# Kernel tuning notes

Hardware: AMD Instinct MI355X
Metric: run time of the kernel (lower is better)

The kernel has to match this reference:

```python
import jax, jax.numpy as jnp
import numpy as np
from jax import lax

B, N, K = 8, 4096, 64
RATIO1, R1 = 0.5, 0.2
RATIO2, R2 = 0.25, 0.4
SA1_DIMS = [3, 32, 32, 64]
SA2_DIMS = [64 + 3, 64, 64, 128]
SA3_DIMS = [128 + 3, 128, 256, 512]


def _mlp_params(key, dims, prefix):
    params = {}
    for i, (din, dout) in enumerate(zip(dims[:-1], dims[1:])):
        key, k1 = jax.random.split(key)
        s = 1.0 / np.sqrt(din)
        params[f"{prefix}_w{i}"] = jax.random.uniform(k1, (din, dout), jnp.float32, -s, s)
        params[f"{prefix}_b{i}"] = jnp.zeros((dout,), jnp.float32)
    return params, key


def setup_inputs() -> dict:
    key = jax.random.key(0)
    key, kp = jax.random.split(key)
    inp = {"pos": jax.random.uniform(kp, (B, N, 3), jnp.float32)}  # unit-cube point clouds
    p1, key = _mlp_params(key, SA1_DIMS, "sa1"); inp.update(p1)
    p2, key = _mlp_params(key, SA2_DIMS, "sa2"); inp.update(p2)
    p3, key = _mlp_params(key, SA3_DIMS, "sa3"); inp.update(p3)
    key, k1, k2 = jax.random.split(key, 3)
    s = 1.0 / np.sqrt(512)
    inp["w_mu"] = jax.random.uniform(k1, (512, 32), jnp.float32, -s, s)
    inp["b_mu"] = jnp.zeros((32,), jnp.float32)
    inp["w_lv"] = jax.random.uniform(k2, (512, 32), jnp.float32, -s, s)
    inp["b_lv"] = jnp.zeros((32,), jnp.float32)
    return inp


def _mlp(x, params):
    # PyG MLP semantics (plain_last=True): ReLU on all but the final layer.
    for i, (w, b) in enumerate(params):
        x = x @ w + b
        if i < len(params) - 1:
            x = jax.nn.relu(x)
    return x


def _fps(pos, M):
    # Farthest point sampling, deterministic start at index 0. pos: [N,3] -> [M]
    n = pos.shape[0]
    def step(carry, _):
        dist, far = carry
        d = jnp.sum((pos - pos[far]) ** 2, axis=-1)
        dist = jnp.minimum(dist, d)
        return (dist, jnp.argmax(dist).astype(jnp.int32)), far
    _, idx = lax.scan(step, (jnp.full(n, jnp.inf, pos.dtype), jnp.int32(0)), None, length=M)
    return idx


def _sa(x, pos, ratio, r, params):
    # SAModule: FPS -> radius query (K nearest within r) -> gather -> MLP -> masked max
    Nn = pos.shape[1]
    M = int(round(ratio * Nn))
    idx = jax.vmap(lambda p: _fps(p, M))(pos)                 # [B,M]
    centers = jax.vmap(lambda p, i: p[i])(pos, idx)           # [B,M,3]
    d2 = jnp.sum((centers[:, :, None, :] - pos[:, None, :, :]) ** 2, axis=-1)  # [B,M,N]
    neg = jnp.where(d2 <= r * r, -d2, -jnp.inf)
    vals, nbr = lax.top_k(neg, K)                             # [B,M,K]
    mask = vals > -jnp.inf                                    # valid neighbors (self always valid)
    pos_j = jax.vmap(lambda p, i: p[i])(pos, nbr)             # [B,M,K,3]
    rel = pos_j - centers[:, :, None, :]
    if x is None:
        feat = rel
    else:
        x_j = jax.vmap(lambda f, i: f[i])(x, nbr)             # [B,M,K,C]
        feat = jnp.concatenate([x_j, rel], axis=-1)
    h = _mlp(feat, params)                                    # [B,M,K,C']
    h = jnp.where(mask[..., None], h, -jnp.inf)
    out = jnp.max(h, axis=2)                                  # scatter-max aggregation
    out = jnp.where(jnp.isfinite(out), out, 0.0)
    return out, centers


def reference(pos, sa1_w0, sa1_b0, sa1_w1, sa1_b1, sa1_w2, sa1_b2,
              sa2_w0, sa2_b0, sa2_w1, sa2_b1, sa2_w2, sa2_b2,
              sa3_w0, sa3_b0, sa3_w1, sa3_b1, sa3_w2, sa3_b2,
              w_mu, b_mu, w_lv, b_lv):
    p1 = [(sa1_w0, sa1_b0), (sa1_w1, sa1_b1), (sa1_w2, sa1_b2)]
    p2 = [(sa2_w0, sa2_b0), (sa2_w1, sa2_b1), (sa2_w2, sa2_b2)]
    p3 = [(sa3_w0, sa3_b0), (sa3_w1, sa3_b1), (sa3_w2, sa3_b2)]
    x1, pos1 = _sa(None, pos, RATIO1, R1, p1)                 # [B,2048,64]
    x2, pos2 = _sa(x1, pos1, RATIO2, R2, p2)                  # [B,512,128]
    g = _mlp(jnp.concatenate([x2, pos2], axis=-1), p3)        # [B,512,512]
    feat = jnp.max(g, axis=1)                                 # global max pool [B,512]
    mu = feat @ w_mu + b_mu
    log_var = feat @ w_lv + b_lv
    eps = jax.random.normal(jax.random.key(42), mu.shape, mu.dtype)
    z = mu + eps * jnp.exp(0.5 * log_var)
    return (z, mu, log_var)
```

## Files before the change

kernel.cpp:

```cpp
#include <hip/hip_runtime.h>
#include <cstdint>
#include <cstddef>


constexpr int BATCH = 8;
constexpr int NPT0  = 4096;
constexpr int M1    = 2048;
constexpr int M2    = 512;
constexpr int KNB   = 64;
constexpr int CAP   = 1024;
constexpr int NCONS = 248;

constexpr size_t O_WT1S1 = 0;
constexpr size_t O_WT2S1 = 96;
constexpr size_t O_WT3S1 = 1120;
constexpr size_t O_WT1S2 = 3168;
constexpr size_t O_WT2S2 = 7456;
constexpr size_t O_WT3S2 = 11552;
constexpr size_t O_WT1S3 = 19744;
constexpr size_t O_WT2S3 = 36512;
constexpr size_t O_POS1  = 69280;
constexpr size_t O_X1    = 118432;
constexpr size_t O_POS2  = 1167008;
constexpr size_t O_X2    = 1179296;
constexpr size_t O_H2G   = O_X1;
constexpr size_t O_FP    = O_X2;
constexpr size_t O_PROG  = 1703584;

template <int C>
__device__ __forceinline__ int dppmov(int x) {
  return __builtin_amdgcn_update_dpp(x, x, C, 0xF, 0xF, false);
}

__device__ __forceinline__ float wave_fmax_scal(float x) {
  x = fmaxf(x, __int_as_float(dppmov<0x111>(__float_as_int(x))));
  x = fmaxf(x, __int_as_float(dppmov<0x112>(__float_as_int(x))));
  x = fmaxf(x, __int_as_float(dppmov<0x114>(__float_as_int(x))));
  x = fmaxf(x, __int_as_float(dppmov<0x118>(__float_as_int(x))));
  x = fmaxf(x, __int_as_float(dppmov<0x142>(__float_as_int(x))));
  x = fmaxf(x, __int_as_float(dppmov<0x143>(__float_as_int(x))));
  return __int_as_float(__builtin_amdgcn_readlane(__float_as_int(x), 63));
}

template <int C>
__device__ __forceinline__ void dpp_key_max(uint32_t& lo, uint32_t& hi) {
  uint32_t olo = (uint32_t)dppmov<C>((int)lo);
  uint32_t ohi = (uint32_t)dppmov<C>((int)hi);
  bool bet = (ohi > hi) || (ohi == hi && olo > lo);
  lo = bet ? olo : lo;
  hi = bet ? ohi : hi;
}
__device__ __forceinline__ void wave_key_max_scal(uint32_t& lo, uint32_t& hi) {
  dpp_key_max<0x111>(lo, hi);
  dpp_key_max<0x112>(lo, hi);
  dpp_key_max<0x114>(lo, hi);
  dpp_key_max<0x118>(lo, hi);
  dpp_key_max<0x142>(lo, hi);
  dpp_key_max<0x143>(lo, hi);
  lo = (uint32_t)__builtin_amdgcn_readlane((int)lo, 63);
  hi = (uint32_t)__builtin_amdgcn_readlane((int)hi, 63);
}
template <int C>
__device__ __forceinline__ void dpp_key_min(uint32_t& lo, uint32_t& hi) {
  uint32_t olo = (uint32_t)dppmov<C>((int)lo);
  uint32_t ohi = (uint32_t)dppmov<C>((int)hi);
  bool bet = (ohi < hi) || (ohi == hi && olo < lo);
  lo = bet ? olo : lo;
  hi = bet ? ohi : hi;
}
__device__ __forceinline__ void wave_key_min_scal(uint32_t& lo, uint32_t& hi) {
  dpp_key_min<0x111>(lo, hi);
  dpp_key_min<0x112>(lo, hi);
  dpp_key_min<0x114>(lo, hi);
  dpp_key_min<0x118>(lo, hi);
  dpp_key_min<0x142>(lo, hi);
  dpp_key_min<0x143>(lo, hi);
  lo = (uint32_t)__builtin_amdgcn_readlane((int)lo, 63);
  hi = (uint32_t)__builtin_amdgcn_readlane((int)hi, 63);
}

__device__ __forceinline__ void wave_lds_fence() {
  asm volatile("s_waitcnt lgkmcnt(0)" ::: "memory");
}

__device__ __forceinline__ uint32_t rotl32(uint32_t x, int d) {
  return (x << d) | (x >> (32 - d));
}

__device__ __forceinline__ void threefry_0_42(uint32_t c0, uint32_t c1,
                                              uint32_t& o0, uint32_t& o1) {
  const uint32_t k0 = 0u, k1 = 42u;
  const uint32_t ks[3] = {k0, k1, k0 ^ k1 ^ 0x1BD11BDAu};
  uint32_t x0 = c0 + ks[0];
  uint32_t x1 = c1 + ks[1];
  const int R0[4] = {13, 15, 26, 6};
  const int R1[4] = {17, 29, 16, 24};
  #pragma unroll
  for (int g = 0; g < 5; ++g) {
    const int* R = (g & 1) ? R1 : R0;
    #pragma unroll
    for (int r = 0; r < 4; ++r) {
      x0 += x1;
      x1 = rotl32(x1, R[r]);
      x1 ^= x0;
    }
    x0 += ks[(g + 1) % 3];
    x1 += ks[(g + 2) % 3] + (uint32_t)(g + 1);
  }
  o0 = x0; o1 = x1;
}

__device__ __forceinline__ float erfinv_xla(float x) {
  float w = -log1pf(-x * x);
  float p;
  if (w < 5.0f) {
    w = w - 2.5f;
    p = 2.81022636e-08f;
    p = fmaf(p, w, 3.43273939e-07f);
    p = fmaf(p, w, -3.5233877e-06f);
    p = fmaf(p, w, -4.39150654e-06f);
    p = fmaf(p, w, 0.00021858087f);
    p = fmaf(p, w, -0.00125372503f);
    p = fmaf(p, w, -0.00417768164f);
    p = fmaf(p, w, 0.246640727f);
    p = fmaf(p, w, 1.50140941f);
  } else {
    w = sqrtf(w) - 3.0f;
    p = -0.000200214257f;
    p = fmaf(p, w, 0.000100950558f);
    p = fmaf(p, w, 0.00134934322f);
    p = fmaf(p, w, -0.00367342844f);
    p = fmaf(p, w, 0.00573950773f);
    p = fmaf(p, w, -0.0076224613f);
    p = fmaf(p, w, 0.00943887047f);
    p = fmaf(p, w, 1.00167406f);
    p = fmaf(p, w, 2.83297682f);
  }
  return p * x;
}

__global__ __launch_bounds__(256) void prep_transpose(
    const float* __restrict__ a0, const float* __restrict__ a1,
    const float* __restrict__ a2, const float* __restrict__ a3,
    const float* __restrict__ a4, const float* __restrict__ a5,
    const float* __restrict__ a6, const float* __restrict__ a7,
    float* __restrict__ ws) {
  int u0 = blockIdx.x * 256 + threadIdx.x;
  if (u0 < 16) ((int*)(ws + O_PROG))[u0] = 0;
  int u = u0;
  if (u < 96)    { ws[O_WT1S1 + u] = a0[(u % 3)   * 32  + u / 3];   return; } u -= 96;
  if (u < 1024)  { ws[O_WT2S1 + u] = a1[(u % 32)  * 32  + u / 32];  return; } u -= 1024;
  if (u < 2048)  { ws[O_WT3S1 + u] = a2[(u % 32)  * 64  + u / 32];  return; } u -= 2048;
  if (u < 4288)  { ws[O_WT1S2 + u] = a3[(u % 67)  * 64  + u / 67];  return; } u -= 4288;
  if (u < 4096)  { ws[O_WT2S2 + u] = a4[(u % 64)  * 64  + u / 64];  return; } u -= 4096;
  if (u < 8192)  { ws[O_WT3S2 + u] = a5[(u % 64)  * 128 + u / 64];  return; } u -= 8192;
  if (u < 16768) { ws[O_WT1S3 + u] = a6[(u % 131) * 128 + u / 131]; return; } u -= 16768;
  if (u < 32768) { ws[O_WT2S3 + u] = a7[(u % 128) * 256 + u / 128]; return; }
}

template <int N, int M, int T>
__device__ __forceinline__ void fps_body(const float* __restrict__ pos,
                                         float* __restrict__ centers,
                                         int* __restrict__ prog,
                                         char* smem, int b) {
  constexpr int PPT = N / T;
  constexpr int NW  = T / 64;
  float* px = (float*)smem;
  float* py = px + N;
  float* pz = py + N;
  int*    tags  = (int*)(pz + N);
  float4* slotA = (float4*)(tags + 16);
  float*  slotZ = (float*)(slotA + 2 * NW);
  const int tid  = threadIdx.x;
  const int lane = tid & 63;
  const int wid  = tid >> 6;
  const float* pb = pos + (size_t)b * N * 3;

  if (tid < 16) tags[tid] = -1;

  float mx[PPT], my[PPT], mz[PPT], md[PPT];
  #pragma unroll
  for (int s = 0; s < PPT; ++s) {
    int i = s * T + tid;
    float x = pb[i * 3 + 0], y = pb[i * 3 + 1], z = pb[i * 3 + 2];
    px[i] = x; py[i] = y; pz[i] = z;
    mx[s] = x; my[s] = y; mz[s] = z;
    md[s] = __builtin_inff();
  }
  __syncthreads();

  float cx = px[0], cy = py[0], cz = pz[0];
  float* cb = centers + (size_t)b * M * 3;

  for (int m = 0; m < M; ++m) {
    if (tid == 0) {
      cb[m * 3 + 0] = cx; cb[m * 3 + 1] = cy; cb[m * 3 + 2] = cz;
      if ((m & 63) == 63)
        __hip_atomic_store(prog + b, m + 1, __ATOMIC_RELEASE,
                           __HIP_MEMORY_SCOPE_AGENT);
    }
    float bv = -1.0f;
    int   bi = 0x7FFFFFFF;
    {
      #pragma clang fp contract(off)
      #pragma unroll
      for (int s = 0; s < PPT; ++s) {
        float dx = mx[s] - cx, dy = my[s] - cy, dz = mz[s] - cz;
        float d = (dx * dx + dy * dy) + dz * dz;
        float nd = fminf(md[s], d);
        md[s] = nd;
        if (nd > bv) { bv = nd; bi = s * T + tid; }
      }
    }
    uint32_t klo = ~(uint32_t)bi;
    uint32_t khi = __float_as_uint(bv);
    wave_key_max_scal(klo, khi);
    int p = (int)~klo;

    float wx = px[p], wy = py[p], wz = pz[p];
    const int par = (m & 1) * NW;
    if (lane == 0) {
      slotA[par + wid] =
          make_float4(__uint_as_float(khi), __uint_as_float(klo), wx, wy);
      slotZ[par + wid] = wz;
    }
    __builtin_amdgcn_fence(__ATOMIC_RELEASE, "workgroup");
    if (lane == 0)
      __hip_atomic_store(&tags[wid], m, __ATOMIC_RELAXED,
                         __HIP_MEMORY_SCOPE_WORKGROUP);
    for (;;) {
      int tmin = __hip_atomic_load(&tags[0], __ATOMIC_RELAXED,
                                   __HIP_MEMORY_SCOPE_WORKGROUP);
      #pragma unroll
      for (int w = 1; w < NW; ++w) {
        int tw = __hip_atomic_load(&tags[w], __ATOMIC_RELAXED,
                                   __HIP_MEMORY_SCOPE_WORKGROUP);
        tmin = min(tmin, tw);
      }
      if (tmin >= m) break;
    }
    __builtin_amdgcn_fence(__ATOMIC_ACQUIRE, "workgroup");

    float4 aw0 = slotA[par + 0];
    uint32_t Khi = __float_as_uint(aw0.x), Klo = __float_as_uint(aw0.y);
    float sx = aw0.z, sy = aw0.w, sz = slotZ[par + 0];
    #pragma unroll
    for (int w = 1; w < NW; ++w) {
      float4 aw = slotA[par + w];
      float zz = slotZ[par + w];
      uint32_t ohi = __float_as_uint(aw.x), olo = __float_as_uint(aw.y);
      bool bet = (ohi > Khi) || (ohi == Khi && olo > Klo);
      Khi = bet ? ohi : Khi;
      Klo = bet ? olo : Klo;
      sx  = bet ? aw.z : sx;
      sy  = bet ? aw.w : sy;
      sz  = bet ? zz   : sz;
    }
    cx = sx; cy = sy; cz = sz;
  }
}

template <int NPTS, int DF, int D1, int D2, int DOUT, int MM>
__device__ __forceinline__ void sa_body(
    const float* __restrict__ pts, const float* __restrict__ feats,
    const float* __restrict__ centers, float* __restrict__ outf,
    const float* __restrict__ wt1, const float* __restrict__ bz1,
    const float* __restrict__ wt2, const float* __restrict__ bz2,
    const float* __restrict__ wt3, const float* __restrict__ bz3,
    float r2max, int* __restrict__ prog, char* smem) {
  constexpr int DIN = DF + 3;
  const int lane = threadIdx.x & 63;
  const int wid  = threadIdx.x >> 6;
  const int g0 = ((int)blockIdx.x - 8) * 8 + wid;
  const int b = g0 & 7;
  const int mbase = g0 >> 3;
  float* sd = (float*)(smem + wid * 8192);
  int*   si = (int*)(smem + wid * 8192 + 4096);
  const float* pb = pts + (size_t)b * NPTS * 3;

  for (int m = mbase; m < MM; m += NCONS) {
    for (;;) {
      int r = 0;
      if (lane == 0)
        r = __hip_atomic_load(prog + b, __ATOMIC_ACQUIRE,
                              __HIP_MEMORY_SCOPE_AGENT);
      r = __builtin_amdgcn_readfirstlane(r);
      if (r > m) break;
      if (m - r > 128) __builtin_amdgcn_s_sleep(64);
      else             __builtin_amdgcn_s_sleep(4);
    }
    __builtin_amdgcn_fence(__ATOMIC_ACQUIRE, "agent");

    const float* cc = centers + ((size_t)b * MM + m) * 3;
    const float cx = cc[0], cy = cc[1], cz = cc[2];

    int cnt = 0;
    const unsigned long long ltmask = (1ull << lane) - 1ull;
    for (int base = 0; base < NPTS; base += 64) {
      int i = base + lane;
      float x3 = pb[i * 3 + 0], y3 = pb[i * 3 + 1], z3 = pb[i * 3 + 2];
      float d2;
      {
        #pragma clang fp contract(off)
        float dx = cx - x3, dy = cy - y3, dz = cz - z3;
        d2 = (dx * dx + dy * dy) + dz * dz;
      }
      bool inr = (d2 <= r2max);
      unsigned long long mk = __ballot(inr);
      int p = cnt + (int)__popcll(mk & ltmask);
      if (inr && p < CAP) { sd[p] = d2; si[p] = i; }
      cnt += (int)__popcll(mk);
    }
    if (cnt > CAP) cnt = CAP;
    wave_lds_fence();

    int my_nbr = -1;
    if (cnt <= KNB) {
      my_nbr = (lane < cnt) ? si[lane] : -1;
    } else {
      constexpr int SMAX = CAP / 64;
      float rd[SMAX];
      #pragma unroll
      for (int s = 0; s < SMAX; ++s) {
        rd[s] = __builtin_inff();
        if (s * 64 < cnt) {
          int q = s * 64 + lane;
          if (q < cnt) rd[s] = sd[q];
        }
      }
      for (int k = 0; k < KNB; ++k) {
        float bv = rd[0];
        int   bp = lane;
        #pragma unroll
        for (int s = 1; s < SMAX; ++s) {
          if (s * 64 < cnt) {
            if (rd[s] < bv) { bv = rd[s]; bp = s * 64 + lane; }
          }
        }
        uint32_t klo = (uint32_t)bp;
        uint32_t khi = __float_as_uint(bv);
        wave_key_min_scal(klo, khi);
        int bpw = (int)klo;
        if (lane == k) my_nbr = si[bpw];
        int wl = bpw & 63, wsl = bpw >> 6;
        #pragma unroll
        for (int s = 0; s < SMAX; ++s) {
          if (s * 64 < cnt) {
            rd[s] = (lane == wl && s == wsl) ? __builtin_inff() : rd[s];
          }
        }
      }
    }
    const bool valid = (my_nbr >= 0);
    const int safeN = valid ? my_nbr : 0;

    float rel[3];
    {
      const float* pr = pb + (size_t)safeN * 3;
      rel[0] = pr[0] - cx; rel[1] = pr[1] - cy; rel[2] = pr[2] - cz;
    }
    float xin[DF > 0 ? DF : 1];
    if constexpr (DF > 0) {
      const float* xr = feats + ((size_t)b * NPTS + safeN) * DF;
      #pragma unroll
      for (int i = 0; i < DF; i += 4) {
        float4 v = *reinterpret_cast<const float4*>(xr + i);
        xin[i] = v.x; xin[i + 1] = v.y; xin[i + 2] = v.z; xin[i + 3] = v.w;
      }
    }

    float h1[D1];
    for (int c = 0; c < D1; c += 4) {
      const float* w0 = wt1 + (c + 0) * DIN;
      const float* w1 = wt1 + (c + 1) * DIN;
      const float* w2 = wt1 + (c + 2) * DIN;
      const float* w3 = wt1 + (c + 3) * DIN;
      float a0 = bz1[c + 0], a1 = bz1[c + 1], a2 = bz1[c + 2], a3 = bz1[c + 3];
      if constexpr (DF > 0) {
        #pragma unroll
        for (int i = 0; i < DF; ++i) {
          a0 = fmaf(xin[i], w0[i], a0);
          a1 = fmaf(xin[i], w1[i], a1);
          a2 = fmaf(xin[i], w2[i], a2);
          a3 = fmaf(xin[i], w3[i], a3);
        }
      }
      #pragma unroll
      for (int r = 0; r < 3; ++r) {
        a0 = fmaf(rel[r], w0[DF + r], a0);
        a1 = fmaf(rel[r], w1[DF + r], a1);
        a2 = fmaf(rel[r], w2[DF + r], a2);
        a3 = fmaf(rel[r], w3[DF + r], a3);
      }
      h1[c + 0] = fmaxf(a0, 0.0f);
      h1[c + 1] = fmaxf(a1, 0.0f);
      h1[c + 2] = fmaxf(a2, 0.0f);
      h1[c + 3] = fmaxf(a3, 0.0f);
    }

    float h2[D2];
    for (int c = 0; c < D2; c += 4) {
      const float* w0 = wt2 + (c + 0) * D1;
      const float* w1 = wt2 + (c + 1) * D1;
      const float* w2 = wt2 + (c + 2) * D1;
      const float* w3 = wt2 + (c + 3) * D1;
      float a0 = bz2[c + 0], a1 = bz2[c + 1], a2 = bz2[c + 2], a3 = bz2[c + 3];
      #pragma unroll
      for (int i = 0; i < D1; ++i) {
        a0 = fmaf(h1[i], w0[i], a0);
        a1 = fmaf(h1[i], w1[i], a1);
        a2 = fmaf(h1[i], w2[i], a2);
        a3 = fmaf(h1[i], w3[i], a3);
      }
      h2[c + 0] = fmaxf(a0, 0.0f);
      h2[c + 1] = fmaxf(a1, 0.0f);
      h2[c + 2] = fmaxf(a2, 0.0f);
      h2[c + 3] = fmaxf(a3, 0.0f);
    }

    float* orow = outf + ((size_t)b * MM + m) * DOUT;
    #pragma unroll
    for (int u = 0; u < DOUT / 64; ++u) {
      float outv = 0.0f;
      for (int ccb = 0; ccb < 64; ccb += 4) {
        const int c = u * 64 + ccb;
        const float* w0 = wt3 + (c + 0) * D2;
        const float* w1 = wt3 + (c + 1) * D2;
        const float* w2 = wt3 + (c + 2) * D2;
        const float* w3 = wt3 + (c + 3) * D2;
        float a0 = bz3[c + 0], a1 = bz3[c + 1], a2 = bz3[c + 2], a3 = bz3[c + 3];
        #pragma unroll
        for (int i = 0; i < D2; ++i) {
          a0 = fmaf(h2[i], w0[i], a0);
          a1 = fmaf(h2[i], w1[i], a1);
          a2 = fmaf(h2[i], w2[i], a2);
          a3 = fmaf(h2[i], w3[i], a3);
        }
        const float NI = -__builtin_inff();
        float s0 = wave_fmax_scal(valid ? a0 : NI);
        float s1 = wave_fmax_scal(valid ? a1 : NI);
        float s2 = wave_fmax_scal(valid ? a2 : NI);
        float s3 = wave_fmax_scal(valid ? a3 : NI);
        if (lane == ccb + 0) outv = s0;
        if (lane == ccb + 1) outv = s1;
        if (lane == ccb + 2) outv = s2;
        if (lane == ccb + 3) outv = s3;
      }
      orow[u * 64 + lane] = outv;
    }
  }
}

__global__ __launch_bounds__(512, 2) void stageA_kernel(
    const float* __restrict__ pos, float* __restrict__ ws,
    const float* __restrict__ bz1, const float* __restrict__ bz2,
    const float* __restrict__ bz3) {
  extern __shared__ char smem[];
  int* prog = (int*)(ws + O_PROG);
  if (blockIdx.x < 8) {
    asm volatile("s_setprio 3");
    fps_body<NPT0, M1, 512>(pos, ws + O_POS1, prog, smem, blockIdx.x);
  } else {
    sa_body<NPT0, 0, 32, 32, 64, M1>(
        pos, nullptr, ws + O_POS1, ws + O_X1,
        ws + O_WT1S1, bz1, ws + O_WT2S1, bz2, ws + O_WT3S1, bz3,
        0.04f, prog, smem);
  }
}

__global__ __launch_bounds__(512, 2) void stageB_kernel(
    float* __restrict__ ws,
    const float* __restrict__ bz1, const float* __restrict__ bz2,
    const float* __restrict__ bz3) {
  extern __shared__ char smem[];
  int* prog = (int*)(ws + O_PROG) + 8;
  if (blockIdx.x < 8) {
    asm volatile("s_setprio 3");
    fps_body<M1, M2, 512>(ws + O_POS1, ws + O_POS2, prog, smem, blockIdx.x);
  } else {
    sa_body<M1, 64, 64, 64, 128, M2>(
        ws + O_POS1, ws + O_X1, ws + O_POS2, ws + O_X2,
        ws + O_WT1S2, bz1, ws + O_WT2S2, bz2, ws + O_WT3S2, bz3,
        0.16f, prog, smem);
  }
}

__global__ __launch_bounds__(256) void sa3_l12_kernel(
    const float* __restrict__ x2, const float* __restrict__ pos2,
    const float* __restrict__ wt1, const float* __restrict__ bz1,
    const float* __restrict__ wt2, const float* __restrict__ bz2,
    float* __restrict__ h2g) {
  __shared__ float H[64 * 132];
  const int tid = threadIdx.x;
  const int lane = tid & 63, w = tid >> 6;
  const int b = blockIdx.x >> 3, tile = blockIdx.x & 7;
  const int pt = tile * 64 + lane;
  const float* xrow = x2 + ((size_t)b * 512 + pt) * 128;
  float* hrow = H + lane * 132;
  const int c0 = w * 32;

  float f[64];
  #pragma unroll
  for (int i = 0; i < 64; i += 4) {
    float4 v = *reinterpret_cast<const float4*>(xrow + i);
    f[i] = v.x; f[i + 1] = v.y; f[i + 2] = v.z; f[i + 3] = v.w;
  }
  for (int c = c0; c < c0 + 32; ++c) {
    const float* wv = wt1 + c * 131;
    float acc = bz1[c];
    #pragma unroll
    for (int i = 0; i < 64; ++i) acc = fmaf(f[i], wv[i], acc);
    hrow[c] = acc;
  }
  #pragma unroll
  for (int i = 0; i < 64; i += 4) {
    float4 v = *reinterpret_cast<const float4*>(xrow + 64 + i);
    f[i] = v.x; f[i + 1] = v.y; f[i + 2] = v.z; f[i + 3] = v.w;
  }
  float q0, q1, q2;
  {
    const float* pr = pos2 + ((size_t)b * 512 + pt) * 3;
    q0 = pr[0]; q1 = pr[1]; q2 = pr[2];
  }
  for (int c = c0; c < c0 + 32; ++c) {
    const float* wv = wt1 + c * 131 + 64;
    float acc = hrow[c];
    #pragma unroll
    for (int i = 0; i < 64; ++i) acc = fmaf(f[i], wv[i], acc);
    acc = fmaf(q0, wv[64], acc);
    acc = fmaf(q1, wv[65], acc);
    acc = fmaf(q2, wv[66], acc);
    hrow[c] = fmaxf(acc, 0.0f);
  }
  __syncthreads();

  float h[128];
  #pragma unroll
  for (int i = 0; i < 128; i += 4) {
    float4 v = *reinterpret_cast<const float4*>(hrow + i);
    h[i] = v.x; h[i + 1] = v.y; h[i + 2] = v.z; h[i + 3] = v.w;
  }
  float* grow = h2g + ((size_t)b * 512 + pt) * 256;
  const int c1 = w * 64;
  for (int c = c1; c < c1 + 64; ++c) {
    const float* wv = wt2 + c * 128;
    float acc = bz2[c];
    #pragma unroll
    for (int i = 0; i < 128; ++i) acc = fmaf(h[i], wv[i], acc);
    grow[c] = fmaxf(acc, 0.0f);
  }
}

__global__ __launch_bounds__(256) void sa3_l3_kernel(
    const float* __restrict__ h2g, const float* __restrict__ w3,
    const float* __restrict__ bz3, float* __restrict__ fpart) {
  const int tid = threadIdx.x;
  const int blk = blockIdx.x;
  const int b   = blk >> 6;
  const int t16 = (blk >> 1) & 31;
  const int cb  = blk & 1;
  const int c = cb * 256 + tid;
  const float* hbase = h2g + ((size_t)b * 512 + t16 * 16) * 256;

  float acc[16];
  #pragma unroll
  for (int j = 0; j < 16; ++j) acc[j] = 0.0f;

  for (int i0 = 0; i0 < 256; i0 += 8) {
    float wv[8];
    #pragma unroll
    for (int u = 0; u < 8; ++u) wv[u] = w3[(size_t)(i0 + u) * 512 + c];
    #pragma unroll
    for (int j = 0; j < 16; ++j) {
      const float* hr = hbase + (size_t)j * 256 + i0;
      #pragma unroll
      for (int u = 0; u < 8; ++u) acc[j] = fmaf(hr[u], wv[u], acc[j]);
    }
  }
  float mv = acc[0];
  #pragma unroll
  for (int j = 1; j < 16; ++j) mv = fmaxf(mv, acc[j]);
  fpart[((size_t)b * 32 + t16) * 512 + c] = mv + bz3[c];
}

__global__ __launch_bounds__(64) void final_kernel(
    const float* __restrict__ fpart,
    const float* __restrict__ wmu, const float* __restrict__ bmu,
    const float* __restrict__ wlv, const float* __restrict__ blv,
    float* __restrict__ outp) {
  __shared__ float feat[512];
  const int tid = threadIdx.x;
  const int b = blockIdx.x;
  for (int cidx = tid; cidx < 512; cidx += 64) {
    float mv = fpart[(size_t)b * 32 * 512 + cidx];
    #pragma unroll
    for (int t = 1; t < 32; ++t)
      mv = fmaxf(mv, fpart[((size_t)b * 32 + t) * 512 + cidx]);
    feat[cidx] = mv;
  }
  __syncthreads();
  if (tid < 32) {
    const int c = tid;
    double amu = 0.0, alv = 0.0;
    for (int i = 0; i < 512; ++i) {
      double fv = (double)feat[i];
      amu += fv * (double)wmu[i * 32 + c];
      alv += fv * (double)wlv[i * 32 + c];
    }
    float mu = (float)amu + bmu[c];
    float lv = (float)alv + blv[c];

    uint32_t n = (uint32_t)(b * 32 + c);
    uint32_t o0, o1;
    threefry_0_42(0u, n, o0, o1);
    uint32_t bits = o0 ^ o1;
    float fl = __uint_as_float((bits >> 9) | 0x3f800000u) - 1.0f;
    const float LO = -0.99999994039535522461f;
    float u = fl * 2.0f + LO;
    u = fmaxf(LO, u);
    float eps = 1.4142135623730951f * erfinv_xla(u);
    float z = mu + eps * expf(0.5f * lv);

    outp[b * 32 + c] = z;
    outp[256 + b * 32 + c] = mu;
    outp[512 + b * 32 + c] = lv;
  }
}

extern "C" void kernel_launch(void* const* d_in, const int* in_sizes, int n_in,
                              void* d_out, int out_size, void* d_ws, size_t ws_size,
                              hipStream_t stream) {
  (void)in_sizes; (void)n_in; (void)out_size; (void)ws_size;
  const float* pos  = (const float*)d_in[0];
  const float* s1w0 = (const float*)d_in[1];  const float* s1b0 = (const float*)d_in[2];
  const float* s1w1 = (const float*)d_in[3];  const float* s1b1 = (const float*)d_in[4];
  const float* s1w2 = (const float*)d_in[5];  const float* s1b2 = (const float*)d_in[6];
  const float* s2w0 = (const float*)d_in[7];  const float* s2b0 = (const float*)d_in[8];
  const float* s2w1 = (const float*)d_in[9];  const float* s2b1 = (const float*)d_in[10];
  const float* s2w2 = (const float*)d_in[11]; const float* s2b2 = (const float*)d_in[12];
  const float* s3w0 = (const float*)d_in[13]; const float* s3b0 = (const float*)d_in[14];
  const float* s3w1 = (const float*)d_in[15]; const float* s3b1 = (const float*)d_in[16];
  const float* s3w2 = (const float*)d_in[17]; const float* s3b2 = (const float*)d_in[18];
  const float* wmu  = (const float*)d_in[19]; const float* bmu  = (const float*)d_in[20];
  const float* wlv  = (const float*)d_in[21]; const float* blv  = (const float*)d_in[22];
  float* ws = (float*)d_ws;
  float* out = (float*)d_out;

  prep_transpose<<<271, 256, 0, stream>>>(s1w0, s1w1, s1w2, s2w0, s2w1, s2w2,
                                          s3w0, s3w1, ws);

  stageA_kernel<<<8 + NCONS, 512, 65536, stream>>>(pos, ws, s1b0, s1b1, s1b2);

  stageB_kernel<<<8 + NCONS, 512, 65536, stream>>>(ws, s2b0, s2b1, s2b2);

  sa3_l12_kernel<<<BATCH * 8, 256, 0, stream>>>(
      ws + O_X2, ws + O_POS2, ws + O_WT1S3, s3b0, ws + O_WT2S3, s3b1,
      ws + O_H2G);

  sa3_l3_kernel<<<BATCH * 64, 256, 0, stream>>>(ws + O_H2G, s3w2, s3b2,
                                                ws + O_FP);

  final_kernel<<<BATCH, 64, 0, stream>>>(ws + O_FP, wmu, bmu, wlv, blv, out);
}
```

Measured before the change: 3.781 ms.

## Shrink FPS to 4 waves and batch consumer work into contiguous center chunks

The FPS producer now runs its serial loop with 256 threads (4 waves) instead of 512. All 512 threads still cooperatively stage the point cloud into LDS, then the upper half exit. This aims to cut the per-iteration cross-wave reduction and barrier cost on the serial critical path, at the price of more points per thread. Consumer waves now take contiguous chunks of centers (8 in stage A, 2 in stage B), poll the progress counter once per chunk with a relaxed load followed by an acquire fence, and process the chunk's centers back to back. This reduces polling overhead but delays the start of each chunk until its last center has been produced.

```diff
diff --git a/kernel.cpp b/kernel.cpp
--- a/kernel.cpp
+++ b/kernel.cpp
@@ -158,13 +158,14 @@
   if (u < 32768) { ws[O_WT2S3 + u] = a7[(u % 128) * 256 + u / 128]; return; }
 }
 
-template <int N, int M, int T>
+template <int N, int M>
 __device__ __forceinline__ void fps_body(const float* __restrict__ pos,
                                          float* __restrict__ centers,
                                          int* __restrict__ prog,
                                          char* smem, int b) {
-  constexpr int PPT = N / T;
-  constexpr int NW  = T / 64;
+  constexpr int TP  = 256;
+  constexpr int PPT = N / TP;
+  constexpr int NW  = 4;
   float* px = (float*)smem;
   float* py = px + N;
   float* pz = py + N;
@@ -177,17 +178,21 @@
   const float* pb = pos + (size_t)b * N * 3;
 
   if (tid < 16) tags[tid] = -1;
+  for (int i = tid; i < N; i += 512) {
+    px[i] = pb[i * 3 + 0];
+    py[i] = pb[i * 3 + 1];
+    pz[i] = pb[i * 3 + 2];
+  }
+  __syncthreads();
+  if (tid >= TP) return;
 
   float mx[PPT], my[PPT], mz[PPT], md[PPT];
   #pragma unroll
   for (int s = 0; s < PPT; ++s) {
-    int i = s * T + tid;
-    float x = pb[i * 3 + 0], y = pb[i * 3 + 1], z = pb[i * 3 + 2];
-    px[i] = x; py[i] = y; pz[i] = z;
-    mx[s] = x; my[s] = y; mz[s] = z;
+    int i = s * TP + tid;
+    mx[s] = px[i]; my[s] = py[i]; mz[s] = pz[i];
     md[s] = __builtin_inff();
   }
-  __syncthreads();
 
   float cx = px[0], cy = py[0], cz = pz[0];
   float* cb = centers + (size_t)b * M * 3;
@@ -209,7 +214,7 @@
         float d = (dx * dx + dy * dy) + dz * dz;
         float nd = fminf(md[s], d);
         md[s] = nd;
-        if (nd > bv) { bv = nd; bi = s * T + tid; }
+        if (nd > bv) { bv = nd; bi = s * TP + tid; }
       }
     }
     uint32_t klo = ~(uint32_t)bi;
@@ -260,7 +265,7 @@
   }
 }
 
-template <int NPTS, int DF, int D1, int D2, int DOUT, int MM>
+template <int NPTS, int DF, int D1, int D2, int DOUT, int MM, int CH>
 __device__ __forceinline__ void sa_body(
     const float* __restrict__ pts, const float* __restrict__ feats,
     const float* __restrict__ centers, float* __restrict__ outf,
@@ -269,184 +274,189 @@
     const float* __restrict__ wt3, const float* __restrict__ bz3,
     float r2max, int* __restrict__ prog, char* smem) {
   constexpr int DIN = DF + 3;
+  constexpr int NCHUNK = MM / CH;
   const int lane = threadIdx.x & 63;
   const int wid  = threadIdx.x >> 6;
   const int g0 = ((int)blockIdx.x - 8) * 8 + wid;
   const int b = g0 & 7;
-  const int mbase = g0 >> 3;
+  const int rank = g0 >> 3;
   float* sd = (float*)(smem + wid * 8192);
   int*   si = (int*)(smem + wid * 8192 + 4096);
   const float* pb = pts + (size_t)b * NPTS * 3;
 
-  for (int m = mbase; m < MM; m += NCONS) {
+  for (int chunk = rank; chunk < NCHUNK; chunk += NCONS) {
+    const int m0 = chunk * CH;
+    const int mlast = m0 + CH - 1;
     for (;;) {
       int r = 0;
       if (lane == 0)
-        r = __hip_atomic_load(prog + b, __ATOMIC_ACQUIRE,
+        r = __hip_atomic_load(prog + b, __ATOMIC_RELAXED,
                               __HIP_MEMORY_SCOPE_AGENT);
       r = __builtin_amdgcn_readfirstlane(r);
-      if (r > m) break;
-      if (m - r > 128) __builtin_amdgcn_s_sleep(64);
-      else             __builtin_amdgcn_s_sleep(4);
+      if (r > mlast) break;
+      if (mlast - r > 128) __builtin_amdgcn_s_sleep(64);
+      else                 __builtin_amdgcn_s_sleep(4);
     }
     __builtin_amdgcn_fence(__ATOMIC_ACQUIRE, "agent");
 
-    const float* cc = centers + ((size_t)b * MM + m) * 3;
-    const float cx = cc[0], cy = cc[1], cz = cc[2];
-
-    int cnt = 0;
-    const unsigned long long ltmask = (1ull << lane) - 1ull;
-    for (int base = 0; base < NPTS; base += 64) {
-      int i = base + lane;
-      float x3 = pb[i * 3 + 0], y3 = pb[i * 3 + 1], z3 = pb[i * 3 + 2];
-      float d2;
-      {
-        #pragma clang fp contract(off)
-        float dx = cx - x3, dy = cy - y3, dz = cz - z3;
-        d2 = (dx * dx + dy * dy) + dz * dz;
-      }
-      bool inr = (d2 <= r2max);
-      unsigned long long mk = __ballot(inr);
-      int p = cnt + (int)__popcll(mk & ltmask);
-      if (inr && p < CAP) { sd[p] = d2; si[p] = i; }
-      cnt += (int)__popcll(mk);
-    }
-    if (cnt > CAP) cnt = CAP;
-    wave_lds_fence();
-
-    int my_nbr = -1;
-    if (cnt <= KNB) {
-      my_nbr = (lane < cnt) ? si[lane] : -1;
-    } else {
-      constexpr int SMAX = CAP / 64;
-      float rd[SMAX];
-      #pragma unroll
-      for (int s = 0; s < SMAX; ++s) {
-        rd[s] = __builtin_inff();
-        if (s * 64 < cnt) {
-          int q = s * 64 + lane;
-          if (q < cnt) rd[s] = sd[q];
-        }
-      }
-      for (int k = 0; k < KNB; ++k) {
-        float bv = rd[0];
-        int   bp = lane;
-        #pragma unroll
-        for (int s = 1; s < SMAX; ++s) {
-          if (s * 64 < cnt) {
-            if (rd[s] < bv) { bv = rd[s]; bp = s * 64 + lane; }
-          }
-        }
-        uint32_t klo = (uint32_t)bp;
-        uint32_t khi = __float_as_uint(bv);
-        wave_key_min_scal(klo, khi);
-        int bpw = (int)klo;
-        if (lane == k) my_nbr = si[bpw];
-        int wl = bpw & 63, wsl = bpw >> 6;
+    for (int m = m0; m <= mlast; ++m) {
+      const float* cc = centers + ((size_t)b * MM + m) * 3;
+      const float cx = cc[0], cy = cc[1], cz = cc[2];
+
+      int cnt = 0;
+      const unsigned long long ltmask = (1ull << lane) - 1ull;
+      for (int base = 0; base < NPTS; base += 64) {
+        int i = base + lane;
+        float x3 = pb[i * 3 + 0], y3 = pb[i * 3 + 1], z3 = pb[i * 3 + 2];
+        float d2;
+        {
+          #pragma clang fp contract(off)
+          float dx = cx - x3, dy = cy - y3, dz = cz - z3;
+          d2 = (dx * dx + dy * dy) + dz * dz;
+        }
+        bool inr = (d2 <= r2max);
+        unsigned long long mk = __ballot(inr);
+        int p = cnt + (int)__popcll(mk & ltmask);
+        if (inr && p < CAP) { sd[p] = d2; si[p] = i; }
+        cnt += (int)__popcll(mk);
+      }
+      if (cnt > CAP) cnt = CAP;
+      wave_lds_fence();
+
+      int my_nbr = -1;
+      if (cnt <= KNB) {
+        my_nbr = (lane < cnt) ? si[lane] : -1;
+      } else {
+        constexpr int SMAX = CAP / 64;
+        float rd[SMAX];
         #pragma unroll
         for (int s = 0; s < SMAX; ++s) {
+          rd[s] = __builtin_inff();
           if (s * 64 < cnt) {
-            rd[s] = (lane == wl && s == wsl) ? __builtin_inff() : rd[s];
+            int q = s * 64 + lane;
+            if (q < cnt) rd[s] = sd[q];
           }
         }
-      }
-    }
-    const bool valid = (my_nbr >= 0);
-    const int safeN = valid ? my_nbr : 0;
-
-    float rel[3];
-    {
-      const float* pr = pb + (size_t)safeN * 3;
-      rel[0] = pr[0] - cx; rel[1] = pr[1] - cy; rel[2] = pr[2] - cz;
-    }
-    float xin[DF > 0 ? DF : 1];
-    if constexpr (DF > 0) {
-      const float* xr = feats + ((size_t)b * NPTS + safeN) * DF;
+        for (int k = 0; k < KNB; ++k) {
+          float bv = rd[0];
+          int   bp = lane;
+          #pragma unroll
+          for (int s = 1; s < SMAX; ++s) {
+            if (s * 64 < cnt) {
+              if (rd[s] < bv) { bv = rd[s]; bp = s * 64 + lane; }
+            }
+          }
+          uint32_t klo = (uint32_t)bp;
+          uint32_t khi = __float_as_uint(bv);
+          wave_key_min_scal(klo, khi);
+          int bpw = (int)klo;
+          if (lane == k) my_nbr = si[bpw];
+          int wl = bpw & 63, wsl = bpw >> 6;
+          #pragma unroll
+          for (int s = 0; s < SMAX; ++s) {
+            if (s * 64 < cnt) {
+              rd[s] = (lane == wl && s == wsl) ? __builtin_inff() : rd[s];
+            }
+          }
+        }
+      }
+      const bool valid = (my_nbr >= 0);
+      const int safeN = valid ? my_nbr : 0;
+
+      float rel[3];
+      {
+        const float* pr = pb + (size_t)safeN * 3;
+        rel[0] = pr[0] - cx; rel[1] = pr[1] - cy; rel[2] = pr[2] - cz;
+      }
+      float xin[DF > 0 ? DF : 1];
+      if constexpr (DF > 0) {
+        const float* xr = feats + ((size_t)b * NPTS + safeN) * DF;
+        #pragma unroll
+        for (int i = 0; i < DF; i += 4) {
+          float4 v = *reinterpret_cast<const float4*>(xr + i);
+          xin[i] = v.x; xin[i + 1] = v.y; xin[i + 2] = v.z; xin[i + 3] = v.w;
+        }
+      }
+
+      float h1[D1];
+      for (int c = 0; c < D1; c += 4) {
+        const float* w0 = wt1 + (c + 0) * DIN;
+        const float* w1 = wt1 + (c + 1) * DIN;
+        const float* w2 = wt1 + (c + 2) * DIN;
+        const float* w3 = wt1 + (c + 3) * DIN;
+        float a0 = bz1[c + 0], a1 = bz1[c + 1], a2 = bz1[c + 2], a3 = bz1[c + 3];
+        if constexpr (DF > 0) {
+          #pragma unroll
+          for (int i = 0; i < DF; ++i) {
+            a0 = fmaf(xin[i], w0[i], a0);
+            a1 = fmaf(xin[i], w1[i], a1);
+            a2 = fmaf(xin[i], w2[i], a2);
+            a3 = fmaf(xin[i], w3[i], a3);
+          }
+        }
+        #pragma unroll
+        for (int r = 0; r < 3; ++r) {
+          a0 = fmaf(rel[r], w0[DF + r], a0);
+          a1 = fmaf(rel[r], w1[DF + r], a1);
+          a2 = fmaf(rel[r], w2[DF + r], a2);
+          a3 = fmaf(rel[r], w3[DF + r], a3);
+        }
+        h1[c + 0] = fmaxf(a0, 0.0f);
+        h1[c + 1] = fmaxf(a1, 0.0f);
+        h1[c + 2] = fmaxf(a2, 0.0f);
+        h1[c + 3] = fmaxf(a3, 0.0f);
+      }
+
+      float h2[D2];
+      for (int c = 0; c < D2; c += 4) {
+        const float* w0 = wt2 + (c + 0) * D1;
+        const float* w1 = wt2 + (c + 1) * D1;
+        const float* w2 = wt2 + (c + 2) * D1;
+        const float* w3 = wt2 + (c + 3) * D1;
+        float a0 = bz2[c + 0], a1 = bz2[c + 1], a2 = bz2[c + 2], a3 = bz2[c + 3];
+        #pragma unroll
+        for (int i = 0; i < D1; ++i) {
+          a0 = fmaf(h1[i], w0[i], a0);
+          a1 = fmaf(h1[i], w1[i], a1);
+          a2 = fmaf(h1[i], w2[i], a2);
+          a3 = fmaf(h1[i], w3[i], a3);
+        }
+        h2[c + 0] = fmaxf(a0, 0.0f);
+        h2[c + 1] = fmaxf(a1, 0.0f);
+        h2[c + 2] = fmaxf(a2, 0.0f);
+        h2[c + 3] = fmaxf(a3, 0.0f);
+      }
+
+      float* orow = outf + ((size_t)b * MM + m) * DOUT;
       #pragma unroll
-      for (int i = 0; i < DF; i += 4) {
-        float4 v = *reinterpret_cast<const float4*>(xr + i);
-        xin[i] = v.x; xin[i + 1] = v.y; xin[i + 2] = v.z; xin[i + 3] = v.w;
-      }
-    }
-
-    float h1[D1];
-    for (int c = 0; c < D1; c += 4) {
-      const float* w0 = wt1 + (c + 0) * DIN;
-      const float* w1 = wt1 + (c + 1) * DIN;
-      const float* w2 = wt1 + (c + 2) * DIN;
-      const float* w3 = wt1 + (c + 3) * DIN;
-      float a0 = bz1[c + 0], a1 = bz1[c + 1], a2 = bz1[c + 2], a3 = bz1[c + 3];
-      if constexpr (DF > 0) {
-        #pragma unroll
-        for (int i = 0; i < DF; ++i) {
-          a0 = fmaf(xin[i], w0[i], a0);
-          a1 = fmaf(xin[i], w1[i], a1);
-          a2 = fmaf(xin[i], w2[i], a2);
-          a3 = fmaf(xin[i], w3[i], a3);
-        }
-      }
-      #pragma unroll
-      for (int r = 0; r < 3; ++r) {
-        a0 = fmaf(rel[r], w0[DF + r], a0);
-        a1 = fmaf(rel[r], w1[DF + r], a1);
-        a2 = fmaf(rel[r], w2[DF + r], a2);
-        a3 = fmaf(rel[r], w3[DF + r], a3);
-      }
-      h1[c + 0] = fmaxf(a0, 0.0f);
-      h1[c + 1] = fmaxf(a1, 0.0f);
-      h1[c + 2] = fmaxf(a2, 0.0f);
-      h1[c + 3] = fmaxf(a3, 0.0f);
-    }
-
-    float h2[D2];
-    for (int c = 0; c < D2; c += 4) {
-      const float* w0 = wt2 + (c + 0) * D1;
-      const float* w1 = wt2 + (c + 1) * D1;
-      const float* w2 = wt2 + (c + 2) * D1;
-      const float* w3 = wt2 + (c + 3) * D1;
-      float a0 = bz2[c + 0], a1 = bz2[c + 1], a2 = bz2[c + 2], a3 = bz2[c + 3];
-      #pragma unroll
-      for (int i = 0; i < D1; ++i) {
-        a0 = fmaf(h1[i], w0[i], a0);
-        a1 = fmaf(h1[i], w1[i], a1);
-        a2 = fmaf(h1[i], w2[i], a2);
-        a3 = fmaf(h1[i], w3[i], a3);
-      }
-      h2[c + 0] = fmaxf(a0, 0.0f);
-      h2[c + 1] = fmaxf(a1, 0.0f);
-      h2[c + 2] = fmaxf(a2, 0.0f);
-      h2[c + 3] = fmaxf(a3, 0.0f);
-    }
-
-    float* orow = outf + ((size_t)b * MM + m) * DOUT;
-    #pragma unroll
-    for (int u = 0; u < DOUT / 64; ++u) {
-      float outv = 0.0f;
-      for (int ccb = 0; ccb < 64; ccb += 4) {
-        const int c = u * 64 + ccb;
-        const float* w0 = wt3 + (c + 0) * D2;
-        const float* w1 = wt3 + (c + 1) * D2;
-        const float* w2 = wt3 + (c + 2) * D2;
-        const float* w3 = wt3 + (c + 3) * D2;
-        float a0 = bz3[c + 0], a1 = bz3[c + 1], a2 = bz3[c + 2], a3 = bz3[c + 3];
-        #pragma unroll
-        for (int i = 0; i < D2; ++i) {
-          a0 = fmaf(h2[i], w0[i], a0);
-          a1 = fmaf(h2[i], w1[i], a1);
-          a2 = fmaf(h2[i], w2[i], a2);
-          a3 = fmaf(h2[i], w3[i], a3);
-        }
-        const float NI = -__builtin_inff();
-        float s0 = wave_fmax_scal(valid ? a0 : NI);
-        float s1 = wave_fmax_scal(valid ? a1 : NI);
-        float s2 = wave_fmax_scal(valid ? a2 : NI);
-        float s3 = wave_fmax_scal(valid ? a3 : NI);
-        if (lane == ccb + 0) outv = s0;
-        if (lane == ccb + 1) outv = s1;
-        if (lane == ccb + 2) outv = s2;
-        if (lane == ccb + 3) outv = s3;
-      }
-      orow[u * 64 + lane] = outv;
+      for (int u = 0; u < DOUT / 64; ++u) {
+        float outv = 0.0f;
+        for (int ccb = 0; ccb < 64; ccb += 4) {
+          const int c = u * 64 + ccb;
+          const float* w0 = wt3 + (c + 0) * D2;
+          const float* w1 = wt3 + (c + 1) * D2;
+          const float* w2 = wt3 + (c + 2) * D2;
+          const float* w3 = wt3 + (c + 3) * D2;
+          float a0 = bz3[c + 0], a1 = bz3[c + 1], a2 = bz3[c + 2], a3 = bz3[c + 3];
+          #pragma unroll
+          for (int i = 0; i < D2; ++i) {
+            a0 = fmaf(h2[i], w0[i], a0);
+            a1 = fmaf(h2[i], w1[i], a1);
+            a2 = fmaf(h2[i], w2[i], a2);
+            a3 = fmaf(h2[i], w3[i], a3);
+          }
+          const float NI = -__builtin_inff();
+          float s0 = wave_fmax_scal(valid ? a0 : NI);
+          float s1 = wave_fmax_scal(valid ? a1 : NI);
+          float s2 = wave_fmax_scal(valid ? a2 : NI);
+          float s3 = wave_fmax_scal(valid ? a3 : NI);
+          if (lane == ccb + 0) outv = s0;
+          if (lane == ccb + 1) outv = s1;
+          if (lane == ccb + 2) outv = s2;
+          if (lane == ccb + 3) outv = s3;
+        }
+        orow[u * 64 + lane] = outv;
+      }
     }
   }
 }
@@ -459,9 +469,9 @@
   int* prog = (int*)(ws + O_PROG);
   if (blockIdx.x < 8) {
     asm volatile("s_setprio 3");
-    fps_body<NPT0, M1, 512>(pos, ws + O_POS1, prog, smem, blockIdx.x);
+    fps_body<NPT0, M1>(pos, ws + O_POS1, prog, smem, blockIdx.x);
   } else {
-    sa_body<NPT0, 0, 32, 32, 64, M1>(
+    sa_body<NPT0, 0, 32, 32, 64, M1, 8>(
         pos, nullptr, ws + O_POS1, ws + O_X1,
         ws + O_WT1S1, bz1, ws + O_WT2S1, bz2, ws + O_WT3S1, bz3,
         0.04f, prog, smem);
@@ -476,9 +486,9 @@
   int* prog = (int*)(ws + O_PROG) + 8;
   if (blockIdx.x < 8) {
     asm volatile("s_setprio 3");
-    fps_body<M1, M2, 512>(ws + O_POS1, ws + O_POS2, prog, smem, blockIdx.x);
+    fps_body<M1, M2>(ws + O_POS1, ws + O_POS2, prog, smem, blockIdx.x);
   } else {
-    sa_body<M1, 64, 64, 64, 128, M2>(
+    sa_body<M1, 64, 64, 64, 128, M2, 2>(
         ws + O_POS1, ws + O_X1, ws + O_POS2, ws + O_X2,
         ws + O_WT1S2, bz1, ws + O_WT2S2, bz2, ws + O_WT3S2, bz3,
         0.16f, prog, smem);
```

After: 4.163 ms. +10.1%, slower.
